# Kernel tuning notes

Hardware: AMD Instinct MI355X
Metric: run time of the kernel (lower is better)

The kernel has to match this reference:

```python
import jax, jax.numpy as jnp
import numpy as np

MAX_BITS = 256.0  # 2**8


def _quantize_kernel(kern):
    # ConfigurableDense.quantize(): symmetric 8-bit fake-quantization of the kernel.
    # qmin starts at 1e10, qmax at -1e10, so first call uses min/max of kernel.
    qmin = jnp.minimum(jnp.float32(1e10), jnp.min(kern))
    qmax = jnp.maximum(jnp.float32(-1e10), jnp.max(kern))
    s = 2.0 * jnp.maximum(jnp.abs(qmin), jnp.abs(qmax)) / MAX_BITS
    return jnp.round(kern / s) * s


def setup_inputs() -> dict:
    key = jax.random.key(0)
    ks = jax.random.split(key, 9)
    B, S, D_IN, D_MODEL = 4, 2048, 1024, 1024
    sc = 0.02
    return {
        "q": jax.random.normal(ks[0], (B, S, D_IN), jnp.float32),
        "k": jax.random.normal(ks[1], (B, S, D_IN), jnp.float32),
        "v": jax.random.normal(ks[2], (B, S, D_IN), jnp.float32),
        "Wq": jax.random.normal(ks[3], (D_IN, D_MODEL), jnp.float32) * sc,
        "bq": jax.random.normal(ks[4], (D_MODEL,), jnp.float32) * sc,
        "Wk": jax.random.normal(ks[5], (D_IN, D_MODEL), jnp.float32) * sc,
        "bk": jax.random.normal(ks[6], (D_MODEL,), jnp.float32) * sc,
        "Wv": jax.random.normal(ks[7], (D_IN, D_MODEL), jnp.float32) * sc,
        "bv": jax.random.normal(ks[8], (D_MODEL,), jnp.float32) * sc,
    }


def reference(q, k, v, Wq, bq, Wk, bk, Wv, bv):
    # Projections with fake-quantized kernels (ConfigurableDense, activation=None).
    qp = jnp.einsum('bsi,id->bsd', q, _quantize_kernel(Wq)) + bq
    kp = jnp.einsum('bsi,id->bsd', k, _quantize_kernel(Wk)) + bk
    vp = jnp.einsum('bsi,id->bsd', v, _quantize_kernel(Wv)) + bv
    # MovingAverageQuantizers are identity on the first call (steps=0 < warmup).
    dk = jnp.float32(kp.shape[-1])
    logits = jnp.einsum('bqd,bkd->bqk', qp, kp) / jnp.sqrt(dk)  # [B, S, S]
    attn = jax.nn.softmax(logits, axis=-1)
    return jnp.einsum('bqk,bkd->bqd', attn, vp)
```

## Files before the change

kernel.cpp:

```cpp
#include <hip/hip_runtime.h>
#include <stdint.h>


typedef unsigned short ushort_t;
typedef __attribute__((ext_vector_type(8))) short short8;
typedef __bf16 bf16x8 __attribute__((ext_vector_type(8)));
typedef __attribute__((ext_vector_type(4))) float floatx4;
typedef __attribute__((ext_vector_type(8))) int int8v;

__device__ __forceinline__ ushort_t f2bf(float x) {
  unsigned u = __float_as_uint(x);
  unsigned r = (u + 0x7fffu + ((u >> 16) & 1u)) >> 16;
  return (ushort_t)r;
}
__device__ __forceinline__ float bf2f(ushort_t u) {
  return __uint_as_float(((unsigned)u) << 16);
}
__device__ __forceinline__ unsigned char f2fp8(float x) {
  return (unsigned char)(__builtin_amdgcn_cvt_pk_fp8_f32(x, x, 0, false) & 0xff);
}

__device__ __forceinline__ void gl_lds16(const void* g, void* l) {
  __builtin_amdgcn_global_load_lds(
      (const __attribute__((address_space(1))) unsigned int*)g,
      (__attribute__((address_space(3))) unsigned int*)l, 16, 0, 0);
}

#define BM 128
#define BN 128
#define BK 64

template <int CMODE, int SWAP>
__global__ __launch_bounds__(256, 2) void gemm_bt(
    const ushort_t* __restrict__ A, const ushort_t* __restrict__ Bt,
    void* __restrict__ Cv, void* __restrict__ Cv8,
    const float* __restrict__ bias0, const float* __restrict__ bias1,
    const float* __restrict__ bias2, int K, int ldc, float alpha, long strideA,
    long strideB, long strideC) {
  __shared__ __attribute__((aligned(16))) ushort_t sA[BM * BK];
  __shared__ __attribute__((aligned(16))) ushort_t sB[BN * BK];

  const int t = threadIdx.x;
  const int lane = t & 63;
  const int wave = t >> 6;
  const int bm = SWAP ? blockIdx.x : blockIdx.y;
  const int bn = SWAP ? blockIdx.y : blockIdx.x;
  const int bz = blockIdx.z;

  const ushort_t* Ab = A + (long)bz * strideA;
  const ushort_t* Bb = Bt + (long)bz * strideB;

  const long a_row0 = (long)bm * BM;
  const long b_row0 = (long)bn * BN;

  const int crow = t >> 3;
  const int schunk = (t & 7) ^ (crow & 7);

  const ushort_t* gA = Ab + (a_row0 + crow) * (long)K + schunk * 8;
  const ushort_t* gB = Bb + (b_row0 + crow) * (long)K + schunk * 8;

  ushort_t* lA = sA + wave * 512;
  ushort_t* lB = sB + wave * 512;

  floatx4 acc[4][4];
#pragma unroll
  for (int i = 0; i < 4; ++i)
#pragma unroll
    for (int j = 0; j < 4; ++j) acc[i][j] = {0.f, 0.f, 0.f, 0.f};

  const int wm = (wave & 1) * 64;
  const int wn = (wave >> 1) * 64;
  const int fr = lane & 15;
  const int fg = lane >> 4;

  int offA[2][4], offB[2][4];
#pragma unroll
  for (int s = 0; s < 2; ++s)
#pragma unroll
    for (int i = 0; i < 4; ++i) {
      int rowA = wm + i * 16 + fr;
      int rowB = wn + i * 16 + fr;
      int cg = s * 4 + fg;
      offA[s][i] = rowA * BK + ((cg ^ (rowA & 7)) * 8);
      offB[s][i] = rowB * BK + ((cg ^ (rowB & 7)) * 8);
    }

  for (int k0 = 0; k0 < K; k0 += BK) {
#pragma unroll
    for (int i = 0; i < 4; ++i) {
      gl_lds16(gA + (long)i * 32 * K, lA + i * 2048);
      gl_lds16(gB + (long)i * 32 * K, lB + i * 2048);
    }
    gA += BK;
    gB += BK;
    __syncthreads();

#pragma unroll
    for (int s = 0; s < 2; ++s) {
      bf16x8 af[4], bfr[4];
#pragma unroll
      for (int i = 0; i < 4; ++i) {
        af[i] = *(const bf16x8*)&sA[offA[s][i]];
        bfr[i] = *(const bf16x8*)&sB[offB[s][i]];
      }
#pragma unroll
      for (int mi = 0; mi < 4; ++mi)
#pragma unroll
        for (int ni = 0; ni < 4; ++ni)
          acc[mi][ni] = __builtin_amdgcn_mfma_f32_16x16x32_bf16(
              af[mi], bfr[ni], acc[mi][ni], 0, 0, 0);
    }
    __syncthreads();
  }

  const int r0 = fg * 4;
  const int cc = fr;
  const float* bias =
      (CMODE == 3) ? (bz == 0 ? bias0 : (bz == 1 ? bias1 : bias2)) : bias0;
  float* Cz32 = (float*)Cv + (long)bz * strideC;
  unsigned char* C8 = (unsigned char*)Cv8 + (long)bz * 8388608L;
  ushort_t* CvpT = (ushort_t*)Cv;

#pragma unroll
  for (int mi = 0; mi < 4; ++mi) {
#pragma unroll
    for (int ni = 0; ni < 4; ++ni) {
      long gm0 = a_row0 + wm + mi * 16 + r0;
      long gn = b_row0 + wn + ni * 16 + cc;
      float vv[4];
#pragma unroll
      for (int r = 0; r < 4; ++r) {
        vv[r] = acc[mi][ni][r] * alpha;
        if (bias) vv[r] += bias[gn];
      }
      if (CMODE == 2) {
#pragma unroll
        for (int r = 0; r < 4; ++r) Cz32[(gm0 + r) * ldc + gn] = vv[r];
      } else if (CMODE == 3 && bz == 2) {
        long b = gm0 >> 11, s = gm0 & 2047;
        ushort4 u4;
        u4.x = f2bf(vv[0]); u4.y = f2bf(vv[1]);
        u4.z = f2bf(vv[2]); u4.w = f2bf(vv[3]);
        *(ushort4*)&CvpT[b * (2048L * 1024L) + gn * 2048L + s] = u4;
      } else {
#pragma unroll
        for (int r = 0; r < 4; ++r) C8[(gm0 + r) * 1024 + gn] = f2fp8(vv[r]);
      }
    }
  }
}

__global__ __launch_bounds__(256, 2) void qk_fp8(
    const unsigned char* __restrict__ Q8, const unsigned char* __restrict__ K8,
    ushort_t* __restrict__ P) {
  __shared__ __attribute__((aligned(16))) unsigned char sA[128 * 128];
  __shared__ __attribute__((aligned(16))) unsigned char sB[128 * 128];
  const int t = threadIdx.x;
  const int lane = t & 63, wave = t >> 6;
  const int bm = blockIdx.x, bn = blockIdx.y, bz = blockIdx.z;

  const unsigned char* Ab = Q8 + (long)bz * 2097152L + (long)bm * 128 * 1024;
  const unsigned char* Bb = K8 + (long)bz * 2097152L + (long)bn * 128 * 1024;

  const int crow = t >> 3;
  const int schunk = (t & 7) ^ (crow & 7);
  const unsigned char* gA = Ab + crow * 1024 + schunk * 16;
  const unsigned char* gB = Bb + crow * 1024 + schunk * 16;
  unsigned char* lA = sA + wave * 1024;
  unsigned char* lB = sB + wave * 1024;

  floatx4 acc[4][4];
#pragma unroll
  for (int i = 0; i < 4; ++i)
#pragma unroll
    for (int j = 0; j < 4; ++j) acc[i][j] = {0.f, 0.f, 0.f, 0.f};

  const int wm = (wave & 1) * 64;
  const int wn = (wave >> 1) * 64;
  const int fr = lane & 15;
  const int fg = lane >> 4;

  int offA[4][2], offB[4][2];
#pragma unroll
  for (int i = 0; i < 4; ++i) {
    int rA = wm + i * 16 + fr;
    int rB = wn + i * 16 + fr;
    offA[i][0] = rA * 128 + (((2 * fg) ^ (rA & 7)) * 16);
    offA[i][1] = rA * 128 + (((2 * fg + 1) ^ (rA & 7)) * 16);
    offB[i][0] = rB * 128 + (((2 * fg) ^ (rB & 7)) * 16);
    offB[i][1] = rB * 128 + (((2 * fg + 1) ^ (rB & 7)) * 16);
  }

  for (int k0 = 0; k0 < 1024; k0 += 128) {
#pragma unroll
    for (int i = 0; i < 4; ++i) {
      gl_lds16(gA + (long)i * 32 * 1024, lA + i * 4096);
      gl_lds16(gB + (long)i * 32 * 1024, lB + i * 4096);
    }
    gA += 128;
    gB += 128;
    __syncthreads();

    int8v af[4], bfr[4];
#pragma unroll
    for (int i = 0; i < 4; ++i) {
      int4 lo = *(const int4*)&sA[offA[i][0]];
      int4 hi = *(const int4*)&sA[offA[i][1]];
      af[i][0] = lo.x; af[i][1] = lo.y; af[i][2] = lo.z; af[i][3] = lo.w;
      af[i][4] = hi.x; af[i][5] = hi.y; af[i][6] = hi.z; af[i][7] = hi.w;
      int4 lo2 = *(const int4*)&sB[offB[i][0]];
      int4 hi2 = *(const int4*)&sB[offB[i][1]];
      bfr[i][0] = lo2.x; bfr[i][1] = lo2.y; bfr[i][2] = lo2.z; bfr[i][3] = lo2.w;
      bfr[i][4] = hi2.x; bfr[i][5] = hi2.y; bfr[i][6] = hi2.z; bfr[i][7] = hi2.w;
    }
#pragma unroll
    for (int mi = 0; mi < 4; ++mi)
#pragma unroll
      for (int ni = 0; ni < 4; ++ni)
        acc[mi][ni] = __builtin_amdgcn_mfma_scale_f32_16x16x128_f8f6f4(
            af[mi], bfr[ni], acc[mi][ni], 0, 0, 0, 127, 0, 127);
    __syncthreads();
  }

  const int r0 = fg * 4;
  const int cc = fr;
#pragma unroll
  for (int mi = 0; mi < 4; ++mi)
#pragma unroll
    for (int ni = 0; ni < 4; ++ni)
#pragma unroll
      for (int r = 0; r < 4; ++r) {
        long gm = (long)bm * 128 + wm + mi * 16 + r0 + r;
        long gn = (long)bn * 128 + wn + ni * 16 + cc;
        P[(long)bz * 4194304L + gm * 2048 + gn] =
            f2bf(acc[mi][ni][r] * 0.03125f);
      }
}

__global__ __launch_bounds__(256) void absmax_k(
    const float* __restrict__ W0, const float* __restrict__ W1,
    const float* __restrict__ W2, unsigned* __restrict__ outv) {
  const float* W = blockIdx.z == 0 ? W0 : (blockIdx.z == 1 ? W1 : W2);
  float m = 0.f;
  const long n = 1024L * 1024L;
  for (long i = (long)blockIdx.x * blockDim.x + threadIdx.x; i < n;
       i += (long)gridDim.x * blockDim.x)
    m = fmaxf(m, fabsf(W[i]));
  for (int off = 32; off; off >>= 1) m = fmaxf(m, __shfl_xor(m, off));
  __shared__ float red[4];
  int lane = threadIdx.x & 63, wave = threadIdx.x >> 6;
  if (lane == 0) red[wave] = m;
  __syncthreads();
  if (threadIdx.x == 0) {
    m = fmaxf(fmaxf(red[0], red[1]), fmaxf(red[2], red[3]));
    atomicMax(&outv[blockIdx.z], __float_as_uint(m));
  }
}

__global__ __launch_bounds__(256) void quant_w_k(
    const float* __restrict__ W0, const float* __restrict__ W1,
    const float* __restrict__ W2, const unsigned* __restrict__ scales,
    ushort_t* __restrict__ Wt) {
  const int z = blockIdx.z;
  const float* W = z == 0 ? W0 : (z == 1 ? W1 : W2);
  const float s = __uint_as_float(scales[z]) * (1.0f / 128.0f);
  __shared__ float tile[32][33];
  const int tx = threadIdx.x & 31, ty = threadIdx.x >> 5;
  const int k0 = blockIdx.y * 32, n0 = blockIdx.x * 32;
#pragma unroll
  for (int i = 0; i < 4; ++i)
    tile[ty + i * 8][tx] = W[(long)(k0 + ty + i * 8) * 1024 + n0 + tx];
  __syncthreads();
  ushort_t* wt = Wt + (long)z * 1024 * 1024;
#pragma unroll
  for (int i = 0; i < 4; ++i) {
    float w = tile[tx][ty + i * 8];
    float qv = rintf(w / s) * s;
    wt[(long)(n0 + ty + i * 8) * 1024 + k0 + tx] = f2bf(qv);
  }
}

__global__ __launch_bounds__(256) void cast3_k(
    const float* __restrict__ q, const float* __restrict__ k,
    const float* __restrict__ v, ushort_t* __restrict__ qb,
    ushort_t* __restrict__ kb, ushort_t* __restrict__ vb) {
  const int z = blockIdx.z;
  const float4* src = (const float4*)(z == 0 ? q : (z == 1 ? k : v));
  ushort_t* dst = z == 0 ? qb : (z == 1 ? kb : vb);
  const long nv = (4L * 2048 * 1024) / 4;
  for (long i = (long)blockIdx.x * blockDim.x + threadIdx.x; i < nv;
       i += (long)gridDim.x * blockDim.x) {
    float4 f = src[i];
    ushort4 u4;
    u4.x = f2bf(f.x); u4.y = f2bf(f.y); u4.z = f2bf(f.z); u4.w = f2bf(f.w);
    *(ushort4*)(dst + i * 4) = u4;
  }
}

__global__ __launch_bounds__(256) void softmax_k(ushort_t* __restrict__ P) {
  const long row = blockIdx.x;
  ushort_t* p = P + row * 2048;
  const int t = threadIdx.x;
  const int lane = t & 63, wave = t >> 6;
  short8 v8 = *(const short8*)&p[t * 8];
  float x[8];
#pragma unroll
  for (int j = 0; j < 8; ++j) x[j] = bf2f((ushort_t)v8[j]);
  float m = x[0];
#pragma unroll
  for (int j = 1; j < 8; ++j) m = fmaxf(m, x[j]);
  for (int off = 32; off; off >>= 1) m = fmaxf(m, __shfl_xor(m, off));
  __shared__ float rmax[4], rsum[4];
  if (lane == 0) rmax[wave] = m;
  __syncthreads();
  m = fmaxf(fmaxf(rmax[0], rmax[1]), fmaxf(rmax[2], rmax[3]));
  float s = 0.f;
#pragma unroll
  for (int j = 0; j < 8; ++j) {
    x[j] = __expf(x[j] - m);
    s += x[j];
  }
  for (int off = 32; off; off >>= 1) s += __shfl_xor(s, off);
  if (lane == 0) rsum[wave] = s;
  __syncthreads();
  s = rsum[0] + rsum[1] + rsum[2] + rsum[3];
  float inv = 1.0f / s;
  short8 o8;
#pragma unroll
  for (int j = 0; j < 8; ++j) o8[j] = (short)f2bf(x[j] * inv);
  *(short8*)&p[t * 8] = o8;
}

extern "C" void kernel_launch(void* const* d_in, const int* in_sizes, int n_in,
                              void* d_out, int out_size, void* d_ws,
                              size_t ws_size, hipStream_t stream) {
  const float* q = (const float*)d_in[0];
  const float* k = (const float*)d_in[1];
  const float* v = (const float*)d_in[2];
  const float* Wq = (const float*)d_in[3];
  const float* bq = (const float*)d_in[4];
  const float* Wk = (const float*)d_in[5];
  const float* bk = (const float*)d_in[6];
  const float* Wv = (const float*)d_in[7];
  const float* bv = (const float*)d_in[8];
  float* out = (float*)d_out;
  char* ws = (char*)d_ws;

  unsigned* scales = (unsigned*)ws;
  ushort_t* Wt = (ushort_t*)(ws + 256);
  ushort_t* qb = (ushort_t*)(ws + 6291712);
  ushort_t* kb = qb + 8388608;
  ushort_t* vb = kb + 8388608;
  ushort_t* P = qb;
  ushort_t* vpT = (ushort_t*)(ws + 73400576);
  unsigned char* qp8 = (unsigned char*)(ws + 90177792);
  unsigned char* kp8 = (unsigned char*)(ws + 98566400);

  hipMemsetAsync(scales, 0, 64, stream);
  absmax_k<<<dim3(64, 1, 3), 256, 0, stream>>>(Wq, Wk, Wv, scales);
  quant_w_k<<<dim3(32, 32, 3), 256, 0, stream>>>(Wq, Wk, Wv, scales, Wt);
  cast3_k<<<dim3(512, 1, 3), 256, 0, stream>>>(q, k, v, qb, kb, vb);

  gemm_bt<3, 1><<<dim3(64, 8, 3), 256, 0, stream>>>(
      qb, Wt, vpT, qp8, bq, bk, bv, 1024, 1024, 1.0f, 8388608L, 1048576L, 0L);

  qk_fp8<<<dim3(16, 16, 4), 256, 0, stream>>>(qp8, kp8, P);

  softmax_k<<<8192, 256, 0, stream>>>(P);

  gemm_bt<2, 1><<<dim3(16, 8, 4), 256, 0, stream>>>(
      P, vpT, out, nullptr, nullptr, nullptr, nullptr, 2048, 1024, 1.0f,
      4194304L, 2097152L, 2097152L);
}
```

Baseline: 314.5 us.

## Fuse input cast into projection GEMM and split softmax across QK and PV

Result: slower. 462.4 us (+47.0%).

```diff
diff --git a/kernel.cpp b/kernel.cpp
--- a/kernel.cpp
+++ b/kernel.cpp
@@ -19,48 +19,32 @@
 __device__ __forceinline__ unsigned char f2fp8(float x) {
   return (unsigned char)(__builtin_amdgcn_cvt_pk_fp8_f32(x, x, 0, false) & 0xff);
 }
-
 __device__ __forceinline__ void gl_lds16(const void* g, void* l) {
   __builtin_amdgcn_global_load_lds(
       (const __attribute__((address_space(1))) unsigned int*)g,
       (__attribute__((address_space(3))) unsigned int*)l, 16, 0, 0);
 }
 
-#define BM 128
-#define BN 128
-#define BK 64
-
-template <int CMODE, int SWAP>
-__global__ __launch_bounds__(256, 2) void gemm_bt(
-    const ushort_t* __restrict__ A, const ushort_t* __restrict__ Bt,
-    void* __restrict__ Cv, void* __restrict__ Cv8,
-    const float* __restrict__ bias0, const float* __restrict__ bias1,
-    const float* __restrict__ bias2, int K, int ldc, float alpha, long strideA,
-    long strideB, long strideC) {
-  __shared__ __attribute__((aligned(16))) ushort_t sA[BM * BK];
-  __shared__ __attribute__((aligned(16))) ushort_t sB[BN * BK];
-
-  const int t = threadIdx.x;
-  const int lane = t & 63;
-  const int wave = t >> 6;
-  const int bm = SWAP ? blockIdx.x : blockIdx.y;
-  const int bn = SWAP ? blockIdx.y : blockIdx.x;
-  const int bz = blockIdx.z;
-
-  const ushort_t* Ab = A + (long)bz * strideA;
-  const ushort_t* Bb = Bt + (long)bz * strideB;
-
-  const long a_row0 = (long)bm * BM;
-  const long b_row0 = (long)bn * BN;
-
-  const int crow = t >> 3;
-  const int schunk = (t & 7) ^ (crow & 7);
-
-  const ushort_t* gA = Ab + (a_row0 + crow) * (long)K + schunk * 8;
-  const ushort_t* gB = Bb + (b_row0 + crow) * (long)K + schunk * 8;
-
-  ushort_t* lA = sA + wave * 512;
+__global__ __launch_bounds__(256, 2) void proj_gemm(
+    const float* __restrict__ Aq, const float* __restrict__ Ak,
+    const float* __restrict__ Av, const ushort_t* __restrict__ Bt,
+    unsigned char* __restrict__ qp8, unsigned char* __restrict__ kp8,
+    ushort_t* __restrict__ vpT, const float* __restrict__ bq,
+    const float* __restrict__ bk, const float* __restrict__ bv) {
+  __shared__ __attribute__((aligned(16))) ushort_t sA[128 * 64];
+  __shared__ __attribute__((aligned(16))) ushort_t sB[128 * 64];
+  const int t = threadIdx.x, lane = t & 63, wave = t >> 6;
+  const int bm = blockIdx.x, bn = blockIdx.y, bz = blockIdx.z;
+  const float* A = bz == 0 ? Aq : (bz == 1 ? Ak : Av);
+  const float* bias = bz == 0 ? bq : (bz == 1 ? bk : bv);
+  const ushort_t* Bb = Bt + (long)bz * 1048576L;
+  const long a_row0 = (long)bm * 128, b_row0 = (long)bn * 128;
+
+  const int crow = t >> 3, c = t & 7, g = c ^ (crow & 7);
+  const float* gA = A + (a_row0 + crow) * 1024L + g * 8;
+  const ushort_t* gB = Bb + (b_row0 + crow) * 1024L + g * 8;
   ushort_t* lB = sB + wave * 512;
+  const int ldsA = crow * 64 + c * 8;
 
   floatx4 acc[4][4];
 #pragma unroll
@@ -68,31 +52,37 @@
 #pragma unroll
     for (int j = 0; j < 4; ++j) acc[i][j] = {0.f, 0.f, 0.f, 0.f};
 
-  const int wm = (wave & 1) * 64;
-  const int wn = (wave >> 1) * 64;
-  const int fr = lane & 15;
-  const int fg = lane >> 4;
-
+  const int wm = (wave & 1) * 64, wn = (wave >> 1) * 64;
+  const int fr = lane & 15, fg = lane >> 4;
   int offA[2][4], offB[2][4];
 #pragma unroll
   for (int s = 0; s < 2; ++s)
 #pragma unroll
     for (int i = 0; i < 4; ++i) {
-      int rowA = wm + i * 16 + fr;
-      int rowB = wn + i * 16 + fr;
+      int rowA = wm + i * 16 + fr, rowB = wn + i * 16 + fr;
       int cg = s * 4 + fg;
-      offA[s][i] = rowA * BK + ((cg ^ (rowA & 7)) * 8);
-      offB[s][i] = rowB * BK + ((cg ^ (rowB & 7)) * 8);
-    }
-
-  for (int k0 = 0; k0 < K; k0 += BK) {
-#pragma unroll
-    for (int i = 0; i < 4; ++i) {
-      gl_lds16(gA + (long)i * 32 * K, lA + i * 2048);
-      gl_lds16(gB + (long)i * 32 * K, lB + i * 2048);
-    }
-    gA += BK;
-    gB += BK;
+      offA[s][i] = rowA * 64 + ((cg ^ (rowA & 7)) * 8);
+      offB[s][i] = rowB * 64 + ((cg ^ (rowB & 7)) * 8);
+    }
+
+  for (int k0 = 0; k0 < 1024; k0 += 64) {
+#pragma unroll
+    for (int i = 0; i < 4; ++i)
+      gl_lds16(gB + (long)i * 32 * 1024, lB + i * 2048);
+    gB += 64;
+#pragma unroll
+    for (int i = 0; i < 4; ++i) {
+      const float* ga = gA + (long)i * 32 * 1024;
+      float4 f0 = *(const float4*)ga;
+      float4 f1 = *(const float4*)(ga + 4);
+      short8 pk;
+      pk[0] = (short)f2bf(f0.x); pk[1] = (short)f2bf(f0.y);
+      pk[2] = (short)f2bf(f0.z); pk[3] = (short)f2bf(f0.w);
+      pk[4] = (short)f2bf(f1.x); pk[5] = (short)f2bf(f1.y);
+      pk[6] = (short)f2bf(f1.z); pk[7] = (short)f2bf(f1.w);
+      *(short8*)&sA[i * 2048 + ldsA] = pk;
+    }
+    gA += 64;
     __syncthreads();
 
 #pragma unroll
@@ -113,14 +103,8 @@
     __syncthreads();
   }
 
-  const int r0 = fg * 4;
-  const int cc = fr;
-  const float* bias =
-      (CMODE == 3) ? (bz == 0 ? bias0 : (bz == 1 ? bias1 : bias2)) : bias0;
-  float* Cz32 = (float*)Cv + (long)bz * strideC;
-  unsigned char* C8 = (unsigned char*)Cv8 + (long)bz * 8388608L;
-  ushort_t* CvpT = (ushort_t*)Cv;
-
+  const int r0 = fg * 4, cc = fr;
+  unsigned char* C8 = bz == 0 ? qp8 : kp8;
 #pragma unroll
   for (int mi = 0; mi < 4; ++mi) {
 #pragma unroll
@@ -129,19 +113,13 @@
       long gn = b_row0 + wn + ni * 16 + cc;
       float vv[4];
 #pragma unroll
-      for (int r = 0; r < 4; ++r) {
-        vv[r] = acc[mi][ni][r] * alpha;
-        if (bias) vv[r] += bias[gn];
-      }
-      if (CMODE == 2) {
-#pragma unroll
-        for (int r = 0; r < 4; ++r) Cz32[(gm0 + r) * ldc + gn] = vv[r];
-      } else if (CMODE == 3 && bz == 2) {
+      for (int r = 0; r < 4; ++r) vv[r] = acc[mi][ni][r] + bias[gn];
+      if (bz == 2) {
         long b = gm0 >> 11, s = gm0 & 2047;
         ushort4 u4;
         u4.x = f2bf(vv[0]); u4.y = f2bf(vv[1]);
         u4.z = f2bf(vv[2]); u4.w = f2bf(vv[3]);
-        *(ushort4*)&CvpT[b * (2048L * 1024L) + gn * 2048L + s] = u4;
+        *(ushort4*)&vpT[b * (2048L * 1024L) + gn * 2048L + s] = u4;
       } else {
 #pragma unroll
         for (int r = 0; r < 4; ++r) C8[(gm0 + r) * 1024 + gn] = f2fp8(vv[r]);
@@ -152,11 +130,12 @@
 
 __global__ __launch_bounds__(256, 2) void qk_fp8(
     const unsigned char* __restrict__ Q8, const unsigned char* __restrict__ K8,
-    ushort_t* __restrict__ P) {
+    ushort_t* __restrict__ P, float* __restrict__ Mp, float* __restrict__ Lp) {
   __shared__ __attribute__((aligned(16))) unsigned char sA[128 * 128];
   __shared__ __attribute__((aligned(16))) unsigned char sB[128 * 128];
-  const int t = threadIdx.x;
-  const int lane = t & 63, wave = t >> 6;
+  __shared__ float redM[2][128];
+  __shared__ float redS[2][128];
+  const int t = threadIdx.x, lane = t & 63, wave = t >> 6;
   const int bm = blockIdx.x, bn = blockIdx.y, bz = blockIdx.z;
 
   const unsigned char* Ab = Q8 + (long)bz * 2097152L + (long)bm * 128 * 1024;
@@ -175,16 +154,13 @@
 #pragma unroll
     for (int j = 0; j < 4; ++j) acc[i][j] = {0.f, 0.f, 0.f, 0.f};
 
-  const int wm = (wave & 1) * 64;
-  const int wn = (wave >> 1) * 64;
-  const int fr = lane & 15;
-  const int fg = lane >> 4;
+  const int wm = (wave & 1) * 64, wn = (wave >> 1) * 64;
+  const int fr = lane & 15, fg = lane >> 4;
 
   int offA[4][2], offB[4][2];
 #pragma unroll
   for (int i = 0; i < 4; ++i) {
-    int rA = wm + i * 16 + fr;
-    int rB = wn + i * 16 + fr;
+    int rA = wm + i * 16 + fr, rB = wn + i * 16 + fr;
     offA[i][0] = rA * 128 + (((2 * fg) ^ (rA & 7)) * 16);
     offA[i][1] = rA * 128 + (((2 * fg + 1) ^ (rA & 7)) * 16);
     offB[i][0] = rB * 128 + (((2 * fg) ^ (rB & 7)) * 16);
@@ -222,8 +198,57 @@
     __syncthreads();
   }
 
-  const int r0 = fg * 4;
-  const int cc = fr;
+  const float alpha = 0.03125f;
+  const int r0 = fg * 4, cc = fr;
+
+  float mrow[4][4];
+#pragma unroll
+  for (int mi = 0; mi < 4; ++mi)
+#pragma unroll
+    for (int r = 0; r < 4; ++r) {
+      float m = acc[mi][0][r];
+#pragma unroll
+      for (int ni = 1; ni < 4; ++ni) m = fmaxf(m, acc[mi][ni][r]);
+      m = fmaxf(m, __shfl_xor(m, 1));
+      m = fmaxf(m, __shfl_xor(m, 2));
+      m = fmaxf(m, __shfl_xor(m, 4));
+      m = fmaxf(m, __shfl_xor(m, 8));
+      if (cc == 0) redM[wave >> 1][wm + mi * 16 + fg * 4 + r] = m * alpha;
+    }
+  __syncthreads();
+#pragma unroll
+  for (int mi = 0; mi < 4; ++mi)
+#pragma unroll
+    for (int r = 0; r < 4; ++r) {
+      int row = wm + mi * 16 + fg * 4 + r;
+      mrow[mi][r] = fmaxf(redM[0][row], redM[1][row]);
+    }
+#pragma unroll
+  for (int mi = 0; mi < 4; ++mi)
+#pragma unroll
+    for (int r = 0; r < 4; ++r) {
+      float s = 0.f;
+#pragma unroll
+      for (int ni = 0; ni < 4; ++ni)
+        s += __expf(acc[mi][ni][r] * alpha - mrow[mi][r]);
+      s += __shfl_xor(s, 1);
+      s += __shfl_xor(s, 2);
+      s += __shfl_xor(s, 4);
+      s += __shfl_xor(s, 8);
+      if (cc == 0) redS[wave >> 1][wm + mi * 16 + fg * 4 + r] = s;
+    }
+  __syncthreads();
+  if ((wave >> 1) == 0 && cc == 0) {
+#pragma unroll
+    for (int mi = 0; mi < 4; ++mi)
+#pragma unroll
+      for (int r = 0; r < 4; ++r) {
+        int row = wm + mi * 16 + fg * 4 + r;
+        long gr = (long)bz * 2048 + (long)bm * 128 + row;
+        Mp[gr * 16 + bn] = fmaxf(redM[0][row], redM[1][row]);
+        Lp[gr * 16 + bn] = redS[0][row] + redS[1][row];
+      }
+  }
 #pragma unroll
   for (int mi = 0; mi < 4; ++mi)
 #pragma unroll
@@ -232,9 +257,118 @@
       for (int r = 0; r < 4; ++r) {
         long gm = (long)bm * 128 + wm + mi * 16 + r0 + r;
         long gn = (long)bn * 128 + wn + ni * 16 + cc;
-        P[(long)bz * 4194304L + gm * 2048 + gn] =
-            f2bf(acc[mi][ni][r] * 0.03125f);
-      }
+        P[(long)bz * 4194304L + gm * 2048 + gn] = f2bf(acc[mi][ni][r] * alpha);
+      }
+}
+
+__global__ __launch_bounds__(256) void ml_reduce(const float* __restrict__ Mp,
+                                                 const float* __restrict__ Lp,
+                                                 float2* __restrict__ ML) {
+  int row = blockIdx.x * 256 + threadIdx.x;
+  const float* mp = Mp + (long)row * 16;
+  const float* lp = Lp + (long)row * 16;
+  float m = mp[0];
+#pragma unroll
+  for (int j = 1; j < 16; ++j) m = fmaxf(m, mp[j]);
+  float l = 0.f;
+#pragma unroll
+  for (int j = 0; j < 16; ++j) l += lp[j] * __expf(mp[j] - m);
+  ML[row] = make_float2(m, 1.0f / l);
+}
+
+__global__ __launch_bounds__(256, 2) void pv_gemm(
+    const ushort_t* __restrict__ P, const ushort_t* __restrict__ vpT,
+    const float2* __restrict__ ML, float* __restrict__ out) {
+  __shared__ __attribute__((aligned(16))) ushort_t sA[128 * 64];
+  __shared__ __attribute__((aligned(16))) ushort_t sB[128 * 64];
+  const int t = threadIdx.x, lane = t & 63, wave = t >> 6;
+  const int bm = blockIdx.x, bn = blockIdx.y, bz = blockIdx.z;
+  const ushort_t* Ab = P + (long)bz * 4194304L;
+  const ushort_t* Bb = vpT + (long)bz * 2097152L;
+  const long a_row0 = (long)bm * 128, b_row0 = (long)bn * 128;
+
+  const int crow = t >> 3, c = t & 7, g = c ^ (crow & 7);
+  const ushort_t* gA0 = Ab + (a_row0 + crow) * 2048L + g * 8;
+  const ushort_t* gB = Bb + (b_row0 + crow) * 2048L + g * 8;
+  ushort_t* lB = sB + wave * 512;
+  const int ldsA = crow * 64 + c * 8;
+
+  float mrow_s[4];
+#pragma unroll
+  for (int i = 0; i < 4; ++i)
+    mrow_s[i] = ML[(long)bz * 2048 + a_row0 + i * 32 + crow].x;
+
+  floatx4 acc[4][4];
+#pragma unroll
+  for (int i = 0; i < 4; ++i)
+#pragma unroll
+    for (int j = 0; j < 4; ++j) acc[i][j] = {0.f, 0.f, 0.f, 0.f};
+
+  const int wm = (wave & 1) * 64, wn = (wave >> 1) * 64;
+  const int fr = lane & 15, fg = lane >> 4;
+  int offA[2][4], offB[2][4];
+#pragma unroll
+  for (int s = 0; s < 2; ++s)
+#pragma unroll
+    for (int i = 0; i < 4; ++i) {
+      int rowA = wm + i * 16 + fr, rowB = wn + i * 16 + fr;
+      int cg = s * 4 + fg;
+      offA[s][i] = rowA * 64 + ((cg ^ (rowA & 7)) * 8);
+      offB[s][i] = rowB * 64 + ((cg ^ (rowB & 7)) * 8);
+    }
+
+  for (int k0 = 0; k0 < 2048; k0 += 64) {
+#pragma unroll
+    for (int i = 0; i < 4; ++i)
+      gl_lds16(gB + (long)i * 32 * 2048, lB + i * 2048);
+    gB += 64;
+#pragma unroll
+    for (int i = 0; i < 4; ++i) {
+      short8 raw = *(const short8*)(gA0 + (long)i * 32 * 2048 + k0);
+      short8 pk;
+#pragma unroll
+      for (int j = 0; j < 8; ++j) {
+        float x = bf2f((ushort_t)raw[j]);
+        pk[j] = (short)f2bf(__expf(x - mrow_s[i]));
+      }
+      *(short8*)&sA[i * 2048 + ldsA] = pk;
+    }
+    __syncthreads();
+
+#pragma unroll
+    for (int s = 0; s < 2; ++s) {
+      bf16x8 af[4], bfr[4];
+#pragma unroll
+      for (int i = 0; i < 4; ++i) {
+        af[i] = *(const bf16x8*)&sA[offA[s][i]];
+        bfr[i] = *(const bf16x8*)&sB[offB[s][i]];
+      }
+#pragma unroll
+      for (int mi = 0; mi < 4; ++mi)
+#pragma unroll
+        for (int ni = 0; ni < 4; ++ni)
+          acc[mi][ni] = __builtin_amdgcn_mfma_f32_16x16x32_bf16(
+              af[mi], bfr[ni], acc[mi][ni], 0, 0, 0);
+    }
+    __syncthreads();
+  }
+
+  const int r0 = fg * 4, cc = fr;
+#pragma unroll
+  for (int mi = 0; mi < 4; ++mi) {
+    long gm0 = a_row0 + wm + mi * 16 + r0;
+    float il[4];
+#pragma unroll
+    for (int r = 0; r < 4; ++r) il[r] = ML[(long)bz * 2048 + gm0 + r].y;
+#pragma unroll
+    for (int ni = 0; ni < 4; ++ni) {
+      long gn = b_row0 + wn + ni * 16 + cc;
+#pragma unroll
+      for (int r = 0; r < 4; ++r)
+        out[(long)bz * 2097152L + (gm0 + r) * 1024 + gn] =
+            acc[mi][ni][r] * il[r];
+    }
+  }
 }
 
 __global__ __launch_bounds__(256) void absmax_k(
@@ -280,57 +414,6 @@
   }
 }
 
-__global__ __launch_bounds__(256) void cast3_k(
-    const float* __restrict__ q, const float* __restrict__ k,
-    const float* __restrict__ v, ushort_t* __restrict__ qb,
-    ushort_t* __restrict__ kb, ushort_t* __restrict__ vb) {
-  const int z = blockIdx.z;
-  const float4* src = (const float4*)(z == 0 ? q : (z == 1 ? k : v));
-  ushort_t* dst = z == 0 ? qb : (z == 1 ? kb : vb);
-  const long nv = (4L * 2048 * 1024) / 4;
-  for (long i = (long)blockIdx.x * blockDim.x + threadIdx.x; i < nv;
-       i += (long)gridDim.x * blockDim.x) {
-    float4 f = src[i];
-    ushort4 u4;
-    u4.x = f2bf(f.x); u4.y = f2bf(f.y); u4.z = f2bf(f.z); u4.w = f2bf(f.w);
-    *(ushort4*)(dst + i * 4) = u4;
-  }
-}
-
-__global__ __launch_bounds__(256) void softmax_k(ushort_t* __restrict__ P) {
-  const long row = blockIdx.x;
-  ushort_t* p = P + row * 2048;
-  const int t = threadIdx.x;
-  const int lane = t & 63, wave = t >> 6;
-  short8 v8 = *(const short8*)&p[t * 8];
-  float x[8];
-#pragma unroll
-  for (int j = 0; j < 8; ++j) x[j] = bf2f((ushort_t)v8[j]);
-  float m = x[0];
-#pragma unroll
-  for (int j = 1; j < 8; ++j) m = fmaxf(m, x[j]);
-  for (int off = 32; off; off >>= 1) m = fmaxf(m, __shfl_xor(m, off));
-  __shared__ float rmax[4], rsum[4];
-  if (lane == 0) rmax[wave] = m;
-  __syncthreads();
-  m = fmaxf(fmaxf(rmax[0], rmax[1]), fmaxf(rmax[2], rmax[3]));
-  float s = 0.f;
-#pragma unroll
-  for (int j = 0; j < 8; ++j) {
-    x[j] = __expf(x[j] - m);
-    s += x[j];
-  }
-  for (int off = 32; off; off >>= 1) s += __shfl_xor(s, off);
-  if (lane == 0) rsum[wave] = s;
-  __syncthreads();
-  s = rsum[0] + rsum[1] + rsum[2] + rsum[3];
-  float inv = 1.0f / s;
-  short8 o8;
-#pragma unroll
-  for (int j = 0; j < 8; ++j) o8[j] = (short)f2bf(x[j] * inv);
-  *(short8*)&p[t * 8] = o8;
-}
-
 extern "C" void kernel_launch(void* const* d_in, const int* in_sizes, int n_in,
                               void* d_out, int out_size, void* d_ws,
                               size_t ws_size, hipStream_t stream) {
@@ -348,27 +431,21 @@
 
   unsigned* scales = (unsigned*)ws;
   ushort_t* Wt = (ushort_t*)(ws + 256);
-  ushort_t* qb = (ushort_t*)(ws + 6291712);
-  ushort_t* kb = qb + 8388608;
-  ushort_t* vb = kb + 8388608;
-  ushort_t* P = qb;
-  ushort_t* vpT = (ushort_t*)(ws + 73400576);
-  unsigned char* qp8 = (unsigned char*)(ws + 90177792);
-  unsigned char* kp8 = (unsigned char*)(ws + 98566400);
+  float* Mp = (float*)(ws + 256);
+  float* Lp = (float*)(ws + 524544);
+  float2* ML = (float2*)(ws + 1048832);
+  unsigned char* qp8 = (unsigned char*)(ws + 6291712);
+  unsigned char* kp8 = (unsigned char*)(ws + 14680320);
+  ushort_t* vpT = (ushort_t*)(ws + 23068928);
+  ushort_t* P = (ushort_t*)(ws + 39846144);
 
   hipMemsetAsync(scales, 0, 64, stream);
   absmax_k<<<dim3(64, 1, 3), 256, 0, stream>>>(Wq, Wk, Wv, scales);
   quant_w_k<<<dim3(32, 32, 3), 256, 0, stream>>>(Wq, Wk, Wv, scales, Wt);
-  cast3_k<<<dim3(512, 1, 3), 256, 0, stream>>>(q, k, v, qb, kb, vb);
-
-  gemm_bt<3, 1><<<dim3(64, 8, 3), 256, 0, stream>>>(
-      qb, Wt, vpT, qp8, bq, bk, bv, 1024, 1024, 1.0f, 8388608L, 1048576L, 0L);
-
-  qk_fp8<<<dim3(16, 16, 4), 256, 0, stream>>>(qp8, kp8, P);
-
-  softmax_k<<<8192, 256, 0, stream>>>(P);
-
-  gemm_bt<2, 1><<<dim3(16, 8, 4), 256, 0, stream>>>(
-      P, vpT, out, nullptr, nullptr, nullptr, nullptr, 2048, 1024, 1.0f,
-      4194304L, 2097152L, 2097152L);
-}
+
+  proj_gemm<<<dim3(64, 8, 3), 256, 0, stream>>>(q, k, v, Wt, qp8, kp8, vpT, bq,
+                                                bk, bv);
+  qk_fp8<<<dim3(16, 16, 4), 256, 0, stream>>>(qp8, kp8, P, Mp, Lp);
+  ml_reduce<<<dim3(32), 256, 0, stream>>>(Mp, Lp, ML);
+  pv_gemm<<<dim3(16, 8, 4), 256, 0, stream>>>(P, vpT, ML, out);
+}
```
